# Kernel tuning notes

Measured on AMD Instinct MI355X. Metric: run time of the kernel, lower is better.

## Reference

```python
import jax, jax.numpy as jnp
import numpy as np

TABLE_SIZE = 524288  # 2**19
NUM_LEVELS = 16
F_PER_LEVEL = 2
BASE_RES = 16
MAX_RES = 512
BB_MIN, BB_MAX = -1.0, 1.0
N_POINTS = 524288

_b = np.exp(np.log(MAX_RES / BASE_RES) / (NUM_LEVELS - 1))
RESOLUTIONS = np.array([int(np.floor(BASE_RES * _b ** l)) for l in range(NUM_LEVELS)], dtype=np.float32)
PRIMES = np.array([1, 2654435761, 805459861], dtype=np.uint32)
# 8 cube corners (same order as torch source)
OFFSETS = np.array([[0,0,0],[1,0,0],[0,1,0],[0,0,1],[1,1,0],[1,0,1],[0,1,1],[1,1,1]], dtype=np.float32)


def setup_inputs() -> dict:
    key = jax.random.key(0)
    k1, k2 = jax.random.split(key)
    x = jax.random.uniform(k1, (N_POINTS, 3), jnp.float32, -1.0, 1.0)
    tables = jax.random.normal(k2, (NUM_LEVELS, TABLE_SIZE, F_PER_LEVEL), jnp.float32) * 0.01
    return {"x": x, "tables": tables}


def reference(x, tables):
    # normalize to [0,1) using bounding box
    xn = jnp.clip((x - BB_MIN) / (BB_MAX - BB_MIN), 0.0, 1.0 - 1e-6)
    res = jnp.asarray(RESOLUTIONS)                       # [L]
    xs = xn[None] * res[:, None, None]                   # [L,N,3]
    xf = jnp.floor(xs)
    wf = xs - xf                                         # [L,N,3] trilinear fracs
    off = jnp.asarray(OFFSETS)                           # [8,3]
    # integer corner coords; uint32 wrap preserves hash mod 2**19 (power-of-two table)
    corner = xf[:, :, None, :].astype(jnp.uint32) + off[None, None].astype(jnp.uint32)  # [L,N,8,3]
    primes = jnp.asarray(PRIMES)
    h = (corner[..., 0] * primes[0]) ^ (corner[..., 1] * primes[1]) ^ (corner[..., 2] * primes[2])
    idx = (h % jnp.uint32(TABLE_SIZE)).astype(jnp.int32)  # [L,N,8]
    # trilinear weights: prod over xyz of (1-o)*(1-w) + o*w
    w = jnp.prod((1.0 - off)[None, None] * (1.0 - wf[:, :, None, :])
                 + off[None, None] * wf[:, :, None, :], axis=-1)  # [L,N,8]
    # per-level hashed gather: [L,N,8,F]
    feats = jax.vmap(lambda t, i: t[i])(tables, idx)
    interp = jnp.einsum('lnc,lncf->lnf', w, feats)       # [L,N,F]
    n = x.shape[0]
    return jnp.transpose(interp, (1, 0, 2)).reshape(n, NUM_LEVELS * F_PER_LEVEL)
```

## Files before the change

### kernel.cpp

```cpp
#include <hip/hip_runtime.h>
#include <cstdint>
#include <cstring>

namespace {
constexpr uint32_t kTableSize = 524288u;
constexpr uint32_t kTableMask = kTableSize - 1u;
constexpr uint32_t kP1 = 2654435761u;
constexpr uint32_t kP2 = 805459861u;
}

typedef double v2d __attribute__((ext_vector_type(2)));

__constant__ float c_res[16] = {16.f, 20.f, 25.f, 32.f, 40.f, 50.f, 64.f, 80.f,
                                101.f, 128.f, 161.f, 203.f, 256.f, 322.f, 406.f, 512.f};

__device__ __forceinline__ double hash_interp(const float2* __restrict__ tbl,
                                              float px, float py, float pz,
                                              float res)
{
    const float nx = fminf(fmaxf((px + 1.0f) * 0.5f, 0.0f), 0.999999f);
    const float ny = fminf(fmaxf((py + 1.0f) * 0.5f, 0.0f), 0.999999f);
    const float nz = fminf(fmaxf((pz + 1.0f) * 0.5f, 0.0f), 0.999999f);

    const float sx = nx * res, sy = ny * res, sz = nz * res;
    const float fx = floorf(sx), fy = floorf(sy), fz = floorf(sz);
    const float wx = sx - fx, wy = sy - fy, wz = sz - fz;
    const float ixw = 1.0f - wx, iyw = 1.0f - wy, izw = 1.0f - wz;

    const uint32_t cx = (uint32_t)fx;
    const uint32_t cy = (uint32_t)fy;
    const uint32_t cz = (uint32_t)fz;

    const uint32_t hy0 = cy * kP1;    const uint32_t hy1 = hy0 + kP1;
    const uint32_t hz0 = cz * kP2;    const uint32_t hz1 = hz0 + kP2;

    const uint32_t b00 = cx ^ hy0 ^ hz0;
    const uint32_t b10 = cx ^ hy1 ^ hz0;
    const uint32_t b01 = cx ^ hy0 ^ hz1;
    const uint32_t b11 = cx ^ hy1 ^ hz1;

    float2 g0, g1, g2, g3, g4, g5, g6, g7;

    if ((cx & 1u) == 0u) {
        const float* tf = reinterpret_cast<const float*>(tbl);
        {
            const uint32_t ia = b00 & kTableMask;
            const float4 q = *reinterpret_cast<const float4*>(tf + (ia & ~1u) * 2u);
            const bool hi = (ia & 1u);
            g0 = hi ? make_float2(q.z, q.w) : make_float2(q.x, q.y);
            g1 = hi ? make_float2(q.x, q.y) : make_float2(q.z, q.w);
        }
        {
            const uint32_t ia = b10 & kTableMask;
            const float4 q = *reinterpret_cast<const float4*>(tf + (ia & ~1u) * 2u);
            const bool hi = (ia & 1u);
            g2 = hi ? make_float2(q.z, q.w) : make_float2(q.x, q.y);
            g4 = hi ? make_float2(q.x, q.y) : make_float2(q.z, q.w);
        }
        {
            const uint32_t ia = b01 & kTableMask;
            const float4 q = *reinterpret_cast<const float4*>(tf + (ia & ~1u) * 2u);
            const bool hi = (ia & 1u);
            g3 = hi ? make_float2(q.z, q.w) : make_float2(q.x, q.y);
            g5 = hi ? make_float2(q.x, q.y) : make_float2(q.z, q.w);
        }
        {
            const uint32_t ia = b11 & kTableMask;
            const float4 q = *reinterpret_cast<const float4*>(tf + (ia & ~1u) * 2u);
            const bool hi = (ia & 1u);
            g6 = hi ? make_float2(q.z, q.w) : make_float2(q.x, q.y);
            g7 = hi ? make_float2(q.x, q.y) : make_float2(q.z, q.w);
        }
    } else {
        const uint32_t cx1 = cx + 1u;
        g0 = tbl[(b00) & kTableMask];
        g1 = tbl[(cx1 ^ hy0 ^ hz0) & kTableMask];
        g2 = tbl[(b10) & kTableMask];
        g4 = tbl[(cx1 ^ hy1 ^ hz0) & kTableMask];
        g3 = tbl[(b01) & kTableMask];
        g5 = tbl[(cx1 ^ hy0 ^ hz1) & kTableMask];
        g6 = tbl[(b11) & kTableMask];
        g7 = tbl[(cx1 ^ hy1 ^ hz1) & kTableMask];
    }

    const float w0 = (ixw * iyw) * izw;
    const float w1 = (wx  * iyw) * izw;
    const float w2 = (ixw * wy ) * izw;
    const float w3 = (ixw * iyw) * wz;
    const float w4 = (wx  * wy ) * izw;
    const float w5 = (wx  * iyw) * wz;
    const float w6 = (ixw * wy ) * wz;
    const float w7 = (wx  * wy ) * wz;

    float a0 = w0 * g0.x;           float a1 = w0 * g0.y;
    a0 = fmaf(w1, g1.x, a0);        a1 = fmaf(w1, g1.y, a1);
    a0 = fmaf(w2, g2.x, a0);        a1 = fmaf(w2, g2.y, a1);
    a0 = fmaf(w3, g3.x, a0);        a1 = fmaf(w3, g3.y, a1);
    a0 = fmaf(w4, g4.x, a0);        a1 = fmaf(w4, g4.y, a1);
    a0 = fmaf(w5, g5.x, a0);        a1 = fmaf(w5, g5.y, a1);
    a0 = fmaf(w6, g6.x, a0);        a1 = fmaf(w6, g6.y, a1);
    a0 = fmaf(w7, g7.x, a0);        a1 = fmaf(w7, g7.y, a1);

    float2 r = make_float2(a0, a1);
    double rd;
    memcpy(&rd, &r, sizeof(rd));
    return rd;
}

__device__ __forceinline__ void load_xyz(const float* __restrict__ x, uint32_t p,
                                         float& px, float& py, float& pz)
{
    px = __builtin_nontemporal_load(x + p * 3u + 0u);
    py = __builtin_nontemporal_load(x + p * 3u + 1u);
    pz = __builtin_nontemporal_load(x + p * 3u + 2u);
}

__global__ __launch_bounds__(256) void fine_kernel(
    const float* __restrict__ x,
    const float* __restrict__ tables,
    double* __restrict__ wsrow,
    int n_points)
{
    const uint32_t xcd = blockIdx.x & 7u;
    const uint32_t j   = blockIdx.x >> 3;
    const uint32_t l   = 8u + xcd;
    const uint32_t p   = j * 256u + threadIdx.x;
    if (p >= (uint32_t)n_points) return;

    float px, py, pz;
    load_xyz(x, p, px, py, pz);

    const float2* __restrict__ tbl =
        reinterpret_cast<const float2*>(tables) + (size_t)l * kTableSize;

    const double rd = hash_interp(tbl, px, py, pz, c_res[l]);
    __builtin_nontemporal_store(rd, wsrow + (size_t)xcd * (uint32_t)n_points + p);
}

__global__ __launch_bounds__(256) void coarse_big_kernel(
    const float* __restrict__ x,
    const float* __restrict__ tables,
    double* __restrict__ ws,
    int n_points, int n_quarter)
{
    const uint32_t s = blockIdx.x & 7u;
    const uint32_t j = blockIdx.x >> 3;
    const uint32_t l = (s < 4u) ? 7u : 6u;
    const uint32_t q = s & 3u;
    const uint32_t base = q * (uint32_t)n_quarter;
    const uint32_t lim  = min(base + (uint32_t)n_quarter, (uint32_t)n_points);
    const uint32_t p = base + j * 256u + threadIdx.x;
    if (p >= lim) return;

    float px, py, pz;
    load_xyz(x, p, px, py, pz);

    const float2* __restrict__ tbl =
        reinterpret_cast<const float2*>(tables) + (size_t)l * kTableSize;

    const double rd = hash_interp(tbl, px, py, pz, c_res[l]);
    __builtin_nontemporal_store(rd, ws + (size_t)l * (uint32_t)n_points + p);
}

__global__ __launch_bounds__(256) void coarse_small_kernel(
    const float* __restrict__ x,
    const float* __restrict__ tables,
    double* __restrict__ ws,
    int n_points, int n_quarter)
{
    const uint32_t s = blockIdx.x % 24u;
    const uint32_t j = blockIdx.x / 24u;
    const uint32_t l = s >> 2;
    const uint32_t q = s & 3u;
    const uint32_t base = q * (uint32_t)n_quarter;
    const uint32_t lim  = min(base + (uint32_t)n_quarter, (uint32_t)n_points);
    const uint32_t p = base + j * 256u + threadIdx.x;
    if (p >= lim) return;

    float px, py, pz;
    load_xyz(x, p, px, py, pz);

    const float2* __restrict__ tbl =
        reinterpret_cast<const float2*>(tables) + (size_t)l * kTableSize;

    const double rd = hash_interp(tbl, px, py, pz, c_res[l]);
    __builtin_nontemporal_store(rd, ws + (size_t)l * (uint32_t)n_points + p);
}

__global__ __launch_bounds__(256) void merge_full_kernel(
    const double* __restrict__ ws,
    double* __restrict__ out,
    int n_points)
{
    __shared__ double tile[32][17];
    const uint32_t t  = threadIdx.x;
    const uint32_t p0 = blockIdx.x * 32u;

    #pragma unroll
    for (uint32_t r = 0; r < 2; ++r) {
        const uint32_t lvl = r * 8u + (t >> 5);
        const uint32_t pi  = t & 31u;
        const uint32_t p   = p0 + pi;
        double v = 0.0;
        if (p < (uint32_t)n_points)
            v = __builtin_nontemporal_load(ws + (size_t)lvl * (uint32_t)n_points + p);
        tile[pi][lvl] = v;
    }
    __syncthreads();
    {
        const uint32_t pi = t >> 3;
        const uint32_t j  = t & 7u;
        const uint32_t p  = p0 + pi;
        if (p < (uint32_t)n_points) {
            v2d v;
            v.x = tile[pi][2u * j + 0u];
            v.y = tile[pi][2u * j + 1u];
            __builtin_nontemporal_store(
                v, reinterpret_cast<v2d*>(out + (size_t)p * 16u) + j);
        }
    }
}

__global__ __launch_bounds__(256) void coarse_kernel_r4(
    const float* __restrict__ x,
    const float* __restrict__ tables,
    double* __restrict__ ws,
    int n_points, int n_half)
{
    const uint32_t s = blockIdx.x & 15u;
    const uint32_t j = blockIdx.x >> 4;
    const uint32_t l    = (s < 8u) ? s : (15u - s);
    const uint32_t base = (s < 8u) ? 0u : (uint32_t)n_half;
    const uint32_t lim  = (s < 8u) ? (uint32_t)n_half : (uint32_t)n_points;
    const uint32_t p = base + j * 256u + threadIdx.x;
    if (p >= lim) return;

    float px, py, pz;
    load_xyz(x, p, px, py, pz);

    const float2* __restrict__ tbl =
        reinterpret_cast<const float2*>(tables) + (size_t)l * kTableSize;

    const double rd = hash_interp(tbl, px, py, pz, c_res[l]);
    __builtin_nontemporal_store(rd, ws + (size_t)l * (uint32_t)n_points + p);
}

__global__ __launch_bounds__(256) void merge_half_kernel(
    const double* __restrict__ ws,
    double* __restrict__ out,
    int n_points, int slot_base)
{
    __shared__ double tile[32][9];
    const uint32_t t  = threadIdx.x;
    const uint32_t p0 = blockIdx.x * 32u;
    {
        const uint32_t lvl = t >> 5;
        const uint32_t pi  = t & 31u;
        const uint32_t p   = p0 + pi;
        double v = 0.0;
        if (p < (uint32_t)n_points)
            v = __builtin_nontemporal_load(ws + (size_t)lvl * (uint32_t)n_points + p);
        tile[pi][lvl] = v;
    }
    __syncthreads();
    {
        const uint32_t lvl = t & 7u;
        const uint32_t pi  = t >> 3;
        const uint32_t p   = p0 + pi;
        if (p < (uint32_t)n_points)
            __builtin_nontemporal_store(tile[pi][lvl],
                                        out + (size_t)p * 16u + (uint32_t)slot_base + lvl);
    }
}

__global__ __launch_bounds__(256) void hashenc_fallback(
    const float* __restrict__ x,
    const float* __restrict__ tables,
    float* __restrict__ out,
    int n_points)
{
    const uint32_t tid = blockIdx.x * 256u + threadIdx.x;
    const uint32_t p = tid >> 4;
    const uint32_t l = tid & 15u;
    if (p >= (uint32_t)n_points) return;

    const float px = x[p * 3u + 0u];
    const float py = x[p * 3u + 1u];
    const float pz = x[p * 3u + 2u];

    const float2* __restrict__ tbl =
        reinterpret_cast<const float2*>(tables) + (size_t)l * kTableSize;
    const double rd = hash_interp(tbl, px, py, pz, c_res[l]);
    __builtin_nontemporal_store(rd, reinterpret_cast<double*>(out) + (size_t)p * 16u + l);
}

extern "C" void kernel_launch(void* const* d_in, const int* in_sizes, int n_in,
                              void* d_out, int out_size, void* d_ws, size_t ws_size,
                              hipStream_t stream) {
    const float* x      = (const float*)d_in[0];
    const float* tables = (const float*)d_in[1];
    float* out          = (float*)d_out;

    const int n_points = in_sizes[0] / 3;
    const size_t ws16 = (size_t)16 * (size_t)n_points * sizeof(double);
    const size_t ws8  = (size_t)8  * (size_t)n_points * sizeof(double);

    double* ws = (double*)d_ws;

    if (ws_size >= ws16) {
        const int n_quarter = (n_points + 3) / 4;
        const int chunks_n  = (n_points + 255) / 256;
        const int chunks_q  = (n_quarter + 255) / 256;

        fine_kernel<<<chunks_n * 8, 256, 0, stream>>>(
            x, tables, ws + (size_t)8 * (uint32_t)n_points, n_points);
        coarse_big_kernel<<<chunks_q * 8, 256, 0, stream>>>(
            x, tables, ws, n_points, n_quarter);
        coarse_small_kernel<<<chunks_q * 24, 256, 0, stream>>>(
            x, tables, ws, n_points, n_quarter);
        merge_full_kernel<<<(n_points + 31) / 32, 256, 0, stream>>>(
            ws, (double*)out, n_points);
    } else if (ws_size >= ws8) {
        const int n_half = (n_points + 1) / 2;
        const int merge_grid = (n_points + 31) / 32;
        {
            const int chunks = (n_points + 255) / 256;
            fine_kernel<<<chunks * 8, 256, 0, stream>>>(x, tables, ws, n_points);
        }
        merge_half_kernel<<<merge_grid, 256, 0, stream>>>(ws, (double*)out, n_points, 8);
        {
            const int chunks = (n_half + 255) / 256;
            coarse_kernel_r4<<<chunks * 16, 256, 0, stream>>>(x, tables, ws, n_points, n_half);
        }
        merge_half_kernel<<<merge_grid, 256, 0, stream>>>(ws, (double*)out, n_points, 0);
    } else {
        const int total = n_points * 16;
        const int grid = (total + 255) / 256;
        hashenc_fallback<<<grid, 256, 0, stream>>>(x, tables, out, n_points);
    }
}
```

Before: 296.9 us.

## Densify coarse-level hash tables into per-level grid LUT for vectorized corner loads

```diff
diff --git a/kernel.cpp b/kernel.cpp
--- a/kernel.cpp
+++ b/kernel.cpp
@@ -7,12 +7,15 @@
 constexpr uint32_t kTableMask = kTableSize - 1u;
 constexpr uint32_t kP1 = 2654435761u;
 constexpr uint32_t kP2 = 805459861u;
+constexpr int kLutTotal = 1075325;
 }
 
 typedef double v2d __attribute__((ext_vector_type(2)));
 
 __constant__ float c_res[16] = {16.f, 20.f, 25.f, 32.f, 40.f, 50.f, 64.f, 80.f,
                                 101.f, 128.f, 161.f, 203.f, 256.f, 322.f, 406.f, 512.f};
+__constant__ uint32_t c_dim[8]     = {17, 21, 26, 33, 41, 51, 65, 81};
+__constant__ uint32_t c_lut_off[8] = {0, 4913, 14174, 31750, 67687, 136608, 269259, 543884};
 
 __device__ __forceinline__ double hash_interp(const float2* __restrict__ tbl,
                                               float px, float py, float pz,
@@ -115,6 +118,32 @@
     pz = __builtin_nontemporal_load(x + p * 3u + 2u);
 }
 
+__global__ __launch_bounds__(256) void lut_build_kernel(
+    const float* __restrict__ tables,
+    float2* __restrict__ lut,
+    int total)
+{
+    const uint32_t g = blockIdx.x * 256u + threadIdx.x;
+    if (g >= (uint32_t)total) return;
+
+    uint32_t l = 0;
+    #pragma unroll
+    for (int i = 1; i < 8; ++i)
+        if (g >= c_lut_off[i]) l = i;
+
+    const uint32_t cell = g - c_lut_off[l];
+    const uint32_t D = c_dim[l];
+    const uint32_t z = cell / (D * D);
+    const uint32_t rem = cell - z * D * D;
+    const uint32_t y = rem / D;
+    const uint32_t x = rem - y * D;
+
+    const uint32_t h = (x ^ (y * kP1) ^ (z * kP2)) & kTableMask;
+    const float2* __restrict__ tbl =
+        reinterpret_cast<const float2*>(tables) + (size_t)l * kTableSize;
+    lut[g] = tbl[h];
+}
+
 __global__ __launch_bounds__(256) void fine_kernel(
     const float* __restrict__ x,
     const float* __restrict__ tables,
@@ -137,53 +166,67 @@
     __builtin_nontemporal_store(rd, wsrow + (size_t)xcd * (uint32_t)n_points + p);
 }
 
-__global__ __launch_bounds__(256) void coarse_big_kernel(
+__global__ __launch_bounds__(256) void coarse_dense_kernel(
     const float* __restrict__ x,
-    const float* __restrict__ tables,
+    const float2* __restrict__ lut,
     double* __restrict__ ws,
-    int n_points, int n_quarter)
-{
-    const uint32_t s = blockIdx.x & 7u;
+    int n_points)
+{
+    const uint32_t l = blockIdx.x & 7u;
     const uint32_t j = blockIdx.x >> 3;
-    const uint32_t l = (s < 4u) ? 7u : 6u;
-    const uint32_t q = s & 3u;
-    const uint32_t base = q * (uint32_t)n_quarter;
-    const uint32_t lim  = min(base + (uint32_t)n_quarter, (uint32_t)n_points);
-    const uint32_t p = base + j * 256u + threadIdx.x;
-    if (p >= lim) return;
+    const uint32_t p = j * 256u + threadIdx.x;
+    if (p >= (uint32_t)n_points) return;
 
     float px, py, pz;
     load_xyz(x, p, px, py, pz);
 
-    const float2* __restrict__ tbl =
-        reinterpret_cast<const float2*>(tables) + (size_t)l * kTableSize;
-
-    const double rd = hash_interp(tbl, px, py, pz, c_res[l]);
-    __builtin_nontemporal_store(rd, ws + (size_t)l * (uint32_t)n_points + p);
-}
-
-__global__ __launch_bounds__(256) void coarse_small_kernel(
-    const float* __restrict__ x,
-    const float* __restrict__ tables,
-    double* __restrict__ ws,
-    int n_points, int n_quarter)
-{
-    const uint32_t s = blockIdx.x % 24u;
-    const uint32_t j = blockIdx.x / 24u;
-    const uint32_t l = s >> 2;
-    const uint32_t q = s & 3u;
-    const uint32_t base = q * (uint32_t)n_quarter;
-    const uint32_t lim  = min(base + (uint32_t)n_quarter, (uint32_t)n_points);
-    const uint32_t p = base + j * 256u + threadIdx.x;
-    if (p >= lim) return;
-
-    float px, py, pz;
-    load_xyz(x, p, px, py, pz);
-
-    const float2* __restrict__ tbl =
-        reinterpret_cast<const float2*>(tables) + (size_t)l * kTableSize;
-
-    const double rd = hash_interp(tbl, px, py, pz, c_res[l]);
+    const float res = c_res[l];
+    const uint32_t D = c_dim[l];
+    const uint32_t off = c_lut_off[l];
+
+    const float nx = fminf(fmaxf((px + 1.0f) * 0.5f, 0.0f), 0.999999f);
+    const float ny = fminf(fmaxf((py + 1.0f) * 0.5f, 0.0f), 0.999999f);
+    const float nz = fminf(fmaxf((pz + 1.0f) * 0.5f, 0.0f), 0.999999f);
+
+    const float sx = nx * res, sy = ny * res, sz = nz * res;
+    const float fx = floorf(sx), fy = floorf(sy), fz = floorf(sz);
+    const float wx = sx - fx, wy = sy - fy, wz = sz - fz;
+    const float ixw = 1.0f - wx, iyw = 1.0f - wy, izw = 1.0f - wz;
+
+    const uint32_t cx = (uint32_t)fx;
+    const uint32_t cy = (uint32_t)fy;
+    const uint32_t cz = (uint32_t)fz;
+
+    const uint32_t base = off + cx + D * (cy + D * cz);
+    const float* lf = reinterpret_cast<const float*>(lut);
+
+    float4 q00, q10, q01, q11;
+    memcpy(&q00, lf + 2u * base,               16);
+    memcpy(&q10, lf + 2u * (base + D),         16);
+    memcpy(&q01, lf + 2u * (base + D * D),     16);
+    memcpy(&q11, lf + 2u * (base + D + D * D), 16);
+
+    const float w0 = (ixw * iyw) * izw;
+    const float w1 = (wx  * iyw) * izw;
+    const float w2 = (ixw * wy ) * izw;
+    const float w3 = (ixw * iyw) * wz;
+    const float w4 = (wx  * wy ) * izw;
+    const float w5 = (wx  * iyw) * wz;
+    const float w6 = (ixw * wy ) * wz;
+    const float w7 = (wx  * wy ) * wz;
+
+    float a0 = w0 * q00.x;          float a1 = w0 * q00.y;
+    a0 = fmaf(w1, q00.z, a0);       a1 = fmaf(w1, q00.w, a1);
+    a0 = fmaf(w2, q10.x, a0);       a1 = fmaf(w2, q10.y, a1);
+    a0 = fmaf(w3, q01.x, a0);       a1 = fmaf(w3, q01.y, a1);
+    a0 = fmaf(w4, q10.z, a0);       a1 = fmaf(w4, q10.w, a1);
+    a0 = fmaf(w5, q01.z, a0);       a1 = fmaf(w5, q01.w, a1);
+    a0 = fmaf(w6, q11.x, a0);       a1 = fmaf(w6, q11.y, a1);
+    a0 = fmaf(w7, q11.z, a0);       a1 = fmaf(w7, q11.w, a1);
+
+    float2 r = make_float2(a0, a1);
+    double rd;
+    memcpy(&rd, &r, sizeof(rd));
     __builtin_nontemporal_store(rd, ws + (size_t)l * (uint32_t)n_points + p);
 }
 
@@ -307,17 +350,19 @@
 
     double* ws = (double*)d_ws;
 
-    if (ws_size >= ws16) {
-        const int n_quarter = (n_points + 3) / 4;
-        const int chunks_n  = (n_points + 255) / 256;
-        const int chunks_q  = (n_quarter + 255) / 256;
+    if (ws_size >= ws16 && (size_t)out_size * sizeof(float) >= (size_t)kLutTotal * 8u) {
+        const int chunks_n = (n_points + 255) / 256;
+
+        float2* lut = reinterpret_cast<float2*>(out);
+        lut_build_kernel<<<(kLutTotal + 255) / 256, 256, 0, stream>>>(
+            tables, lut, kLutTotal);
 
         fine_kernel<<<chunks_n * 8, 256, 0, stream>>>(
             x, tables, ws + (size_t)8 * (uint32_t)n_points, n_points);
-        coarse_big_kernel<<<chunks_q * 8, 256, 0, stream>>>(
-            x, tables, ws, n_points, n_quarter);
-        coarse_small_kernel<<<chunks_q * 24, 256, 0, stream>>>(
-            x, tables, ws, n_points, n_quarter);
+
+        coarse_dense_kernel<<<chunks_n * 8, 256, 0, stream>>>(
+            x, lut, ws, n_points);
+
         merge_full_kernel<<<(n_points + 31) / 32, 256, 0, stream>>>(
             ws, (double*)out, n_points);
     } else if (ws_size >= ws8) {
```

After: 341.1 us. 1.15x slower.
